# Kernel optimization log

Measured on AMD Instinct MI355X. Metric: run time of the kernel, lower is better.

Reference implementation:

```python
import jax, jax.numpy as jnp
import numpy as np
from jax import lax


def haar_dwt2(x):
    """Single-level 2D Haar (db1) DWT matching pywt sign conventions.
    x: (..., H, W) with H, W even. Returns (cA, cH, cV, cD) each (..., H/2, W/2).
    pywt db1: approx = (x0+x1)/sqrt2, detail = (x0-x1)/sqrt2; dwt2 keys:
    cH='da' (detail axis -2), cV='ad' (detail axis -1).
    """
    a = x[..., 0::2, 0::2]
    b = x[..., 0::2, 1::2]
    c = x[..., 1::2, 0::2]
    d = x[..., 1::2, 1::2]
    cA = (a + b + c + d) * 0.5
    cH = (a + b - c - d) * 0.5
    cV = (a - b + c - d) * 0.5
    cD = (a - b - c + d) * 0.5
    return cA, cH, cV, cD


def wavedec2_level2_array(x):
    """pywt.wavedec2(x, 'db1', level=2) followed by pywt.coeffs_to_array.
    x: (B, C, H, W) -> (B, C, H, W) coefficient array with layout:
      [[ [[cA2, cH2],[cV2, cD2]], cH1 ],
       [ cV1,                     cD1 ]]
    """
    cA1, cH1, cV1, cD1 = haar_dwt2(x)
    cA2, cH2, cV2, cD2 = haar_dwt2(cA1)
    lvl2 = jnp.concatenate([
        jnp.concatenate([cA2, cH2], axis=-1),
        jnp.concatenate([cV2, cD2], axis=-1),
    ], axis=-2)
    top = jnp.concatenate([lvl2, cH1], axis=-1)
    bot = jnp.concatenate([cV1, cD1], axis=-1)
    return jnp.concatenate([top, bot], axis=-2)


def setup_inputs() -> dict:
    key = jax.random.key(0)
    k1, k2, k3 = jax.random.split(key, 3)
    B, C, H = 128, 3, 224
    dim, patch = 768, 16
    x = jax.random.normal(k1, (B, C, H, H), dtype=jnp.float32)
    # Conv2d default init scale ~ 1/sqrt(fan_in)
    fan_in = C * patch * patch
    W = jax.random.normal(k2, (dim, C, patch, patch), dtype=jnp.float32) / np.sqrt(fan_in)
    b = jax.random.normal(k3, (dim,), dtype=jnp.float32) / np.sqrt(fan_in)
    return {"x": x, "W": W, "b": b}


def reference(x, W, b):
    patch = W.shape[-1]
    coeffs = wavedec2_level2_array(x)  # (B, C, H, W)
    y = lax.conv_general_dilated(
        coeffs, W,
        window_strides=(patch, patch),
        padding='VALID',
        dimension_numbers=('NCHW', 'OIHW', 'NCHW'),
    ) + b[None, :, None, None]          # (B, dim, H/p, W/p)
    B, D, Hp, Wp = y.shape
    return y.reshape(B, D, Hp * Wp).transpose(0, 2, 1)  # (B, seq, dim)
```

## Files before the change

kernel.cpp:

```cpp
#include <hip/hip_runtime.h>
#include <stdint.h>

typedef __attribute__((ext_vector_type(8))) __bf16 bf16x8;
typedef __attribute__((ext_vector_type(4))) float f32x4;

__device__ __forceinline__ unsigned short f2bf(float f) {
  union { float f; unsigned int u; } v; v.f = f;
  unsigned int u = v.u;
  return (unsigned short)((u + 0x7fffu + ((u >> 16) & 1u)) >> 16);
}

__device__ __forceinline__ void async_copy16(const void* g, void* s) {
  __builtin_amdgcn_global_load_lds(
      (__attribute__((address_space(1))) void*)const_cast<void*>(g),
      (__attribute__((address_space(3))) void*)s,
      16, 0, 0);
}

#define HAAR(a, bb, cc, dd, oA, oH, oV, oD)                                    \
  oA = 0.5f * ((a + bb) + (cc + dd));                                          \
  oH = 0.5f * ((a + bb) - (cc + dd));                                          \
  oV = 0.5f * ((a - bb) + (cc - dd));                                          \
  oD = 0.5f * ((a - bb) - (cc - dd));

__global__ __launch_bounds__(256) void convw_kernel(const float* __restrict__ W,
                                                    unsigned short* __restrict__ Wb) {
  int i = blockIdx.x * 256 + threadIdx.x;
  float4 v = ((const float4*)W)[i];
  uint2 o;
  o.x = (unsigned int)f2bf(v.x) | ((unsigned int)f2bf(v.y) << 16);
  o.y = (unsigned int)f2bf(v.z) | ((unsigned int)f2bf(v.w) << 16);
  ((uint2*)Wb)[i] = o;
}

__global__ __launch_bounds__(256) void dwt2_kernel(const float* __restrict__ x,
                                                   unsigned short* __restrict__ A) {
  int tid = blockIdx.x * 256 + threadIdx.x;
  int J = tid % 56;
  int t = tid / 56;
  int I = t % 56;
  t /= 56;
  int c = t % 3;
  int b = t / 3;

  const float* xp = x + (((size_t)t * 224 + 4 * I) * 224 + 4 * J);
  float4 r0 = *(const float4*)(xp);
  float4 r1 = *(const float4*)(xp + 224);
  float4 r2 = *(const float4*)(xp + 448);
  float4 r3 = *(const float4*)(xp + 672);

  float A1[2][2], H1[2][2], V1[2][2], D1[2][2];
  HAAR(r0.x, r0.y, r1.x, r1.y, A1[0][0], H1[0][0], V1[0][0], D1[0][0]);
  HAAR(r0.z, r0.w, r1.z, r1.w, A1[0][1], H1[0][1], V1[0][1], D1[0][1]);
  HAAR(r2.x, r2.y, r3.x, r3.y, A1[1][0], H1[1][0], V1[1][0], D1[1][0]);
  HAAR(r2.z, r2.w, r3.z, r3.w, A1[1][1], H1[1][1], V1[1][1], D1[1][1]);

  auto aidx = [&](int y, int xx) -> size_t {
    int mrow = b * 196 + (y >> 4) * 14 + (xx >> 4);
    int k = c * 256 + (y & 15) * 16 + (xx & 15);
    return (size_t)mrow * 768 + (size_t)k;
  };
  auto store2 = [&](int y, int xx, float v0, float v1) {
    unsigned int p = (unsigned int)f2bf(v0) | ((unsigned int)f2bf(v1) << 16);
    *(unsigned int*)(A + aidx(y, xx)) = p;
  };

  int y0 = 2 * I, x0 = 2 * J;
  store2(y0,           112 + x0, H1[0][0], H1[0][1]);
  store2(y0 + 1,       112 + x0, H1[1][0], H1[1][1]);
  store2(112 + y0,     x0,       V1[0][0], V1[0][1]);
  store2(112 + y0 + 1, x0,       V1[1][0], V1[1][1]);
  store2(112 + y0,     112 + x0, D1[0][0], D1[0][1]);
  store2(112 + y0 + 1, 112 + x0, D1[1][0], D1[1][1]);

  float vA2, vH2, vV2, vD2;
  HAAR(A1[0][0], A1[0][1], A1[1][0], A1[1][1], vA2, vH2, vV2, vD2);
  A[aidx(I,      J)]      = f2bf(vA2);
  A[aidx(I,      56 + J)] = f2bf(vH2);
  A[aidx(56 + I, J)]      = f2bf(vV2);
  A[aidx(56 + I, 56 + J)] = f2bf(vD2);
}

__global__ __launch_bounds__(256) void gemm_kernel(const unsigned short* __restrict__ A,
                                                   const unsigned short* __restrict__ Bt,
                                                   const float* __restrict__ bias,
                                                   float* __restrict__ C) {
  constexpr int K = 768, N = 768;
  constexpr int NT = 12;
  __shared__ unsigned short As[2][128 * 64];
  __shared__ unsigned short Bs[2][192 * 64];

  const int orig = blockIdx.x;
  const int tile = (orig & 7) * 98 + (orig >> 3);
  const int bm = tile >> 2, bn = tile & 3;
  const int mbase = bm * 128, nbase = bn * 192;

  const int tid = threadIdx.x;
  const int lane = tid & 63;
  const int wave = tid >> 6;
  const int wr = wave >> 1, wc = wave & 1;

  f32x4 acc[4][6] = {};

  const int srow = wave * 8 + (lane >> 3);
  const int kcs = (lane & 7) ^ ((lane >> 3) & 7);
  const unsigned short* gA[4];
  const unsigned short* gB[6];
#pragma unroll
  for (int i = 0; i < 4; ++i) gA[i] = A + (size_t)(mbase + i * 32 + srow) * K + kcs * 8;
#pragma unroll
  for (int j = 0; j < 6; ++j) gB[j] = Bt + (size_t)(nbase + j * 32 + srow) * K + kcs * 8;

  auto stageA = [&](int buf, int kt) {
    char* sa = (char*)As + buf * 16384 + wave * 1024;
    const int ko = kt * 64;
#pragma unroll
    for (int i = 0; i < 4; ++i) async_copy16(gA[i] + ko, sa + i * 4096);
  };
  auto stageB = [&](int buf, int kt) {
    char* sb = (char*)Bs + buf * 24576 + wave * 1024;
    const int ko = kt * 64;
#pragma unroll
    for (int j = 0; j < 6; ++j) async_copy16(gB[j] + ko, sb + j * 4096);
  };

  const int fr = lane & 15;
  const int kq = lane >> 4;
  const int ch0 = ((0 * 4 + kq) ^ (fr & 7)) * 16;
  const int ch1 = ((1 * 4 + kq) ^ (fr & 7)) * 16;

  stageA(0, 0);
  stageB(0, 0);
  asm volatile("s_waitcnt vmcnt(0)" ::: "memory");
  __builtin_amdgcn_s_barrier();

#pragma unroll
  for (int kt = 0; kt < NT; ++kt) {
    const int cb = kt & 1;
    const char* pa = (const char*)As + cb * 16384 + (wr * 64 + fr) * 128;
    const char* pb = (const char*)Bs + cb * 24576 + (wc * 96 + fr) * 128;
    bf16x8 af[4], bv[6];

    if (kt + 1 < NT) stageA(cb ^ 1, kt + 1);
#pragma unroll
    for (int ni = 0; ni < 6; ++ni) bv[ni] = *(const bf16x8*)(pb + ni * 2048 + ch0);
#pragma unroll
    for (int mi = 0; mi < 4; ++mi) af[mi] = *(const bf16x8*)(pa + mi * 2048 + ch0);
    asm volatile("s_waitcnt lgkmcnt(0)" ::: "memory");
    __builtin_amdgcn_sched_barrier(0);
    __builtin_amdgcn_s_setprio(1);
#pragma unroll
    for (int mi = 0; mi < 4; ++mi)
#pragma unroll
      for (int ni = 0; ni < 6; ++ni)
        acc[mi][ni] = __builtin_amdgcn_mfma_f32_16x16x32_bf16(af[mi], bv[ni],
                                                              acc[mi][ni], 0, 0, 0);
    __builtin_amdgcn_s_setprio(0);

    if (kt + 1 < NT) stageB(cb ^ 1, kt + 1);
#pragma unroll
    for (int ni = 0; ni < 6; ++ni) bv[ni] = *(const bf16x8*)(pb + ni * 2048 + ch1);
#pragma unroll
    for (int mi = 0; mi < 4; ++mi) af[mi] = *(const bf16x8*)(pa + mi * 2048 + ch1);
    asm volatile("s_waitcnt lgkmcnt(0)" ::: "memory");
    __builtin_amdgcn_sched_barrier(0);
    __builtin_amdgcn_s_setprio(1);
#pragma unroll
    for (int mi = 0; mi < 4; ++mi)
#pragma unroll
      for (int ni = 0; ni < 6; ++ni)
        acc[mi][ni] = __builtin_amdgcn_mfma_f32_16x16x32_bf16(af[mi], bv[ni],
                                                              acc[mi][ni], 0, 0, 0);
    __builtin_amdgcn_s_setprio(0);

    if (kt + 1 < NT) {
      asm volatile("s_waitcnt vmcnt(0)" ::: "memory");
      __builtin_amdgcn_s_barrier();
    }
  }

  const int rq = lane >> 4;
#pragma unroll
  for (int ni = 0; ni < 6; ++ni) {
    int n = nbase + wc * 96 + ni * 16 + fr;
    float bb = bias[n];
#pragma unroll
    for (int mi = 0; mi < 4; ++mi) {
      int mrow = mbase + wr * 64 + mi * 16 + rq * 4;
      f32x4 v = acc[mi][ni];
#pragma unroll
      for (int j = 0; j < 4; ++j) C[(size_t)(mrow + j) * N + n] = v[j] + bb;
    }
  }
}

extern "C" void kernel_launch(void* const* d_in, const int* in_sizes, int n_in,
                              void* d_out, int out_size, void* d_ws, size_t ws_size,
                              hipStream_t stream) {
  const float* x = (const float*)d_in[0];
  const float* W = (const float*)d_in[1];
  const float* bias = (const float*)d_in[2];
  float* out = (float*)d_out;

  unsigned short* A = (unsigned short*)d_ws;
  unsigned short* Wb = (unsigned short*)((char*)d_ws + 38535168);

  convw_kernel<<<576, 256, 0, stream>>>(W, Wb);
  dwt2_kernel<<<4704, 256, 0, stream>>>(x, A);
  gemm_kernel<<<784, 256, 0, stream>>>(A, Wb, bias, out);
}
```

Baseline: 68.84 us.

## Split Haar DWT into two kernels with 16-byte vectorized stores

The fused two-level DWT kernel is replaced by two kernels. The first computes level 1 and writes the detail bands as 16-byte packed bf16 stores. It also writes cA1 to a bf16 scratch buffer. The second reads that scratch and emits the level-2 bands, again with wide stores. The goal is to replace the scattered 4-byte and 2-byte stores with coalesced 16-byte writes. The costs are an extra launch, a scratch round trip, and cA1 being rounded to bf16 before the second level, which adds precision error.

```diff
diff --git a/kernel.cpp b/kernel.cpp
--- a/kernel.cpp
+++ b/kernel.cpp
@@ -8,6 +8,10 @@
   union { float f; unsigned int u; } v; v.f = f;
   unsigned int u = v.u;
   return (unsigned short)((u + 0x7fffu + ((u >> 16) & 1u)) >> 16);
+}
+__device__ __forceinline__ float bf2f(unsigned int hw) {
+  union { unsigned int u; float f; } v; v.u = hw << 16;
+  return v.f;
 }
 
 __device__ __forceinline__ void async_copy16(const void* g, void* s) {
@@ -16,12 +20,6 @@
       (__attribute__((address_space(3))) void*)s,
       16, 0, 0);
 }
-
-#define HAAR(a, bb, cc, dd, oA, oH, oV, oD)                                    \
-  oA = 0.5f * ((a + bb) + (cc + dd));                                          \
-  oH = 0.5f * ((a + bb) - (cc + dd));                                          \
-  oV = 0.5f * ((a - bb) + (cc - dd));                                          \
-  oD = 0.5f * ((a - bb) - (cc - dd));
 
 __global__ __launch_bounds__(256) void convw_kernel(const float* __restrict__ W,
                                                     unsigned short* __restrict__ Wb) {
@@ -33,52 +31,99 @@
   ((uint2*)Wb)[i] = o;
 }
 
-__global__ __launch_bounds__(256) void dwt2_kernel(const float* __restrict__ x,
+__device__ __forceinline__ size_t aidx(int bc_b, int c, int y, int xx) {
+  int mrow = bc_b * 196 + (y >> 4) * 14 + (xx >> 4);
+  int k = c * 256 + (y & 15) * 16 + (xx & 15);
+  return (size_t)mrow * 768 + (size_t)k;
+}
+
+__device__ __forceinline__ uint4 pack8(const float* v) {
+  uint4 o;
+  o.x = (unsigned int)f2bf(v[0]) | ((unsigned int)f2bf(v[1]) << 16);
+  o.y = (unsigned int)f2bf(v[2]) | ((unsigned int)f2bf(v[3]) << 16);
+  o.z = (unsigned int)f2bf(v[4]) | ((unsigned int)f2bf(v[5]) << 16);
+  o.w = (unsigned int)f2bf(v[6]) | ((unsigned int)f2bf(v[7]) << 16);
+  return o;
+}
+
+__global__ __launch_bounds__(256) void dwt1_kernel(const float* __restrict__ x,
+                                                   unsigned short* __restrict__ A,
+                                                   unsigned short* __restrict__ sc) {
+  int tid = blockIdx.x * 256 + threadIdx.x;
+  int s = tid % 14;
+  int r = tid / 14;
+  int I = r % 112;
+  int t = r / 112;
+  int c = t % 3;
+  int b = t / 3;
+
+  const float* xp = x + ((size_t)t * 224 + 2 * I) * 224 + 16 * s;
+  float4 q0 = ((const float4*)xp)[0], q1 = ((const float4*)xp)[1];
+  float4 q2 = ((const float4*)xp)[2], q3 = ((const float4*)xp)[3];
+  const float* xq = xp + 224;
+  float4 p0 = ((const float4*)xq)[0], p1 = ((const float4*)xq)[1];
+  float4 p2 = ((const float4*)xq)[2], p3 = ((const float4*)xq)[3];
+
+  float r0[16] = {q0.x, q0.y, q0.z, q0.w, q1.x, q1.y, q1.z, q1.w,
+                  q2.x, q2.y, q2.z, q2.w, q3.x, q3.y, q3.z, q3.w};
+  float r1[16] = {p0.x, p0.y, p0.z, p0.w, p1.x, p1.y, p1.z, p1.w,
+                  p2.x, p2.y, p2.z, p2.w, p3.x, p3.y, p3.z, p3.w};
+
+  float A1[8], H[8], V[8], D[8];
+#pragma unroll
+  for (int p = 0; p < 8; ++p) {
+    float a = r0[2 * p], bb = r0[2 * p + 1], cc = r1[2 * p], dd = r1[2 * p + 1];
+    A1[p] = 0.5f * ((a + bb) + (cc + dd));
+    H[p]  = 0.5f * ((a + bb) - (cc + dd));
+    V[p]  = 0.5f * ((a - bb) + (cc - dd));
+    D[p]  = 0.5f * ((a - bb) - (cc - dd));
+  }
+
+  int xx = 8 * s;
+  *(uint4*)(A + aidx(b, c, I, 112 + xx))       = pack8(H);
+  *(uint4*)(A + aidx(b, c, 112 + I, xx))       = pack8(V);
+  *(uint4*)(A + aidx(b, c, 112 + I, 112 + xx)) = pack8(D);
+  *(uint4*)(sc + ((size_t)t * 112 + I) * 112 + xx) = pack8(A1);
+}
+
+__global__ __launch_bounds__(256) void dwt2_kernel(const unsigned short* __restrict__ sc,
                                                    unsigned short* __restrict__ A) {
   int tid = blockIdx.x * 256 + threadIdx.x;
-  int J = tid % 56;
-  int t = tid / 56;
-  int I = t % 56;
-  t /= 56;
+  int s = tid % 7;
+  int r = tid / 7;
+  int I = r % 56;
+  int t = r / 56;
   int c = t % 3;
   int b = t / 3;
 
-  const float* xp = x + (((size_t)t * 224 + 4 * I) * 224 + 4 * J);
-  float4 r0 = *(const float4*)(xp);
-  float4 r1 = *(const float4*)(xp + 224);
-  float4 r2 = *(const float4*)(xp + 448);
-  float4 r3 = *(const float4*)(xp + 672);
-
-  float A1[2][2], H1[2][2], V1[2][2], D1[2][2];
-  HAAR(r0.x, r0.y, r1.x, r1.y, A1[0][0], H1[0][0], V1[0][0], D1[0][0]);
-  HAAR(r0.z, r0.w, r1.z, r1.w, A1[0][1], H1[0][1], V1[0][1], D1[0][1]);
-  HAAR(r2.x, r2.y, r3.x, r3.y, A1[1][0], H1[1][0], V1[1][0], D1[1][0]);
-  HAAR(r2.z, r2.w, r3.z, r3.w, A1[1][1], H1[1][1], V1[1][1], D1[1][1]);
-
-  auto aidx = [&](int y, int xx) -> size_t {
-    int mrow = b * 196 + (y >> 4) * 14 + (xx >> 4);
-    int k = c * 256 + (y & 15) * 16 + (xx & 15);
-    return (size_t)mrow * 768 + (size_t)k;
-  };
-  auto store2 = [&](int y, int xx, float v0, float v1) {
-    unsigned int p = (unsigned int)f2bf(v0) | ((unsigned int)f2bf(v1) << 16);
-    *(unsigned int*)(A + aidx(y, xx)) = p;
-  };
-
-  int y0 = 2 * I, x0 = 2 * J;
-  store2(y0,           112 + x0, H1[0][0], H1[0][1]);
-  store2(y0 + 1,       112 + x0, H1[1][0], H1[1][1]);
-  store2(112 + y0,     x0,       V1[0][0], V1[0][1]);
-  store2(112 + y0 + 1, x0,       V1[1][0], V1[1][1]);
-  store2(112 + y0,     112 + x0, D1[0][0], D1[0][1]);
-  store2(112 + y0 + 1, 112 + x0, D1[1][0], D1[1][1]);
-
-  float vA2, vH2, vV2, vD2;
-  HAAR(A1[0][0], A1[0][1], A1[1][0], A1[1][1], vA2, vH2, vV2, vD2);
-  A[aidx(I,      J)]      = f2bf(vA2);
-  A[aidx(I,      56 + J)] = f2bf(vH2);
-  A[aidx(56 + I, J)]      = f2bf(vV2);
-  A[aidx(56 + I, 56 + J)] = f2bf(vD2);
+  const unsigned short* sp = sc + ((size_t)t * 112 + 2 * I) * 112 + 16 * s;
+  uint4 a0 = *(const uint4*)sp, a1 = *(const uint4*)(sp + 8);
+  uint4 b0 = *(const uint4*)(sp + 112), b1 = *(const uint4*)(sp + 120);
+
+  float r0[16] = {bf2f(a0.x & 0xffff), bf2f(a0.x >> 16), bf2f(a0.y & 0xffff), bf2f(a0.y >> 16),
+                  bf2f(a0.z & 0xffff), bf2f(a0.z >> 16), bf2f(a0.w & 0xffff), bf2f(a0.w >> 16),
+                  bf2f(a1.x & 0xffff), bf2f(a1.x >> 16), bf2f(a1.y & 0xffff), bf2f(a1.y >> 16),
+                  bf2f(a1.z & 0xffff), bf2f(a1.z >> 16), bf2f(a1.w & 0xffff), bf2f(a1.w >> 16)};
+  float r1[16] = {bf2f(b0.x & 0xffff), bf2f(b0.x >> 16), bf2f(b0.y & 0xffff), bf2f(b0.y >> 16),
+                  bf2f(b0.z & 0xffff), bf2f(b0.z >> 16), bf2f(b0.w & 0xffff), bf2f(b0.w >> 16),
+                  bf2f(b1.x & 0xffff), bf2f(b1.x >> 16), bf2f(b1.y & 0xffff), bf2f(b1.y >> 16),
+                  bf2f(b1.z & 0xffff), bf2f(b1.z >> 16), bf2f(b1.w & 0xffff), bf2f(b1.w >> 16)};
+
+  float A2[8], H2[8], V2[8], D2[8];
+#pragma unroll
+  for (int p = 0; p < 8; ++p) {
+    float a = r0[2 * p], bb = r0[2 * p + 1], cc = r1[2 * p], dd = r1[2 * p + 1];
+    A2[p] = 0.5f * ((a + bb) + (cc + dd));
+    H2[p] = 0.5f * ((a + bb) - (cc + dd));
+    V2[p] = 0.5f * ((a - bb) + (cc - dd));
+    D2[p] = 0.5f * ((a - bb) - (cc - dd));
+  }
+
+  int xx = 8 * s;
+  *(uint4*)(A + aidx(b, c, I, xx))           = pack8(A2);
+  *(uint4*)(A + aidx(b, c, I, 56 + xx))      = pack8(H2);
+  *(uint4*)(A + aidx(b, c, 56 + I, xx))      = pack8(V2);
+  *(uint4*)(A + aidx(b, c, 56 + I, 56 + xx)) = pack8(D2);
 }
 
 __global__ __launch_bounds__(256) void gemm_kernel(const unsigned short* __restrict__ A,
@@ -204,8 +249,10 @@
 
   unsigned short* A = (unsigned short*)d_ws;
   unsigned short* Wb = (unsigned short*)((char*)d_ws + 38535168);
+  unsigned short* sc = (unsigned short*)((char*)d_ws + 39714816);
 
   convw_kernel<<<576, 256, 0, stream>>>(W, Wb);
-  dwt2_kernel<<<4704, 256, 0, stream>>>(x, A);
+  dwt1_kernel<<<2352, 256, 0, stream>>>(x, A, sc);
+  dwt2_kernel<<<588, 256, 0, stream>>>(sc, A);
   gemm_kernel<<<784, 256, 0, stream>>>(A, Wb, bias, out);
 }
```

After: 72.24 us. 1.05x slower.
